# Kernel tuning notes

Measured on AMD Instinct MI355X. Metric: run time of the kernel, lower is better.

The kernel has to match this reference:

```python
import jax, jax.numpy as jnp
import numpy as np

SR = 11025.0
NYQ = SR / 2.0
N_OSC = 128
UP_LEN = 24576          # smooth_upsample2 target
TOTAL_SAMPLES = 16384   # noise-bank samples
WINDOW = 32             # (17 - 1) * 2
HOP = 16
FRAMES = 1024
CROP = 4096

# buffers derived from zounds.GeometricScale(20, nyquist-20, 0.05, 128)
CENTERS = jnp.asarray(np.geomspace(20.0, NYQ - 20.0, N_OSC), dtype=jnp.float32)
ERBS = CENTERS * 0.108 + 24.7


def conv1d(x, w, pad):
    # x: [B, Cin, T], w: [Cout, Cin, K]
    return jax.lax.conv_general_dilated(
        x, w, window_strides=(1,), padding=[(pad, pad)],
        dimension_numbers=('NCH', 'OIH', 'NCH'))


def lrelu(x):
    return jax.nn.leaky_relu(x, 0.2)


def setup_inputs() -> dict:
    key = jax.random.key(0)
    ks = jax.random.split(key, 16)
    d = {}
    d['x'] = jax.random.normal(ks[0], (16, 256, 64), jnp.float32)
    # xavier-ish scales: std ~ sqrt(2/(fan_in+fan_out))
    d['w_main0'] = jax.random.normal(ks[1], (512, 256, 1), jnp.float32) * 0.06
    d['w_main1'] = jax.random.normal(ks[2], (512, 512, 3), jnp.float32) * 0.03
    d['w_main2'] = jax.random.normal(ks[3], (512, 512, 3), jnp.float32) * 0.03
    d['w_main3'] = jax.random.normal(ks[4], (512, 512, 3), jnp.float32) * 0.03
    d['w_freq'] = jax.random.normal(ks[5], (256, 512, 1), jnp.float32) * 0.06
    for i in range(4):
        d[f'w_nl{i}'] = jax.random.normal(ks[6 + i], (512, 512, 7), jnp.float32) * 0.02
        d[f'b_nl{i}'] = jnp.zeros((512,), jnp.float32)
    d['w_noise_loud'] = jax.random.normal(ks[10], (17, 512, 1), jnp.float32) * 0.06
    d['noise'] = jax.random.uniform(ks[11], (16, FRAMES, WINDOW), jnp.float32)  # mapped to (-1,1) inside
    return d


def reference(x, w_main0, w_main1, w_main2, w_main3, w_freq,
              w_nl0, b_nl0, w_nl1, b_nl1, w_nl2, b_nl2, w_nl3, b_nl3,
              w_noise_loud, noise):
    B = x.shape[0]
    # ---- main conv stack (all bias-free, leaky_relu 0.2) ----
    h = lrelu(conv1d(x, w_main0, 0))
    h = lrelu(conv1d(h, w_main1, 1))
    h = lrelu(conv1d(h, w_main2, 1))
    h = lrelu(conv1d(h, w_main3, 1))          # [B, 512, 64]

    # ---- per-oscillator loudness & frequency ----
    osc = conv1d(h, w_freq, 0)                # [B, 256, 64]
    l = osc[:, :N_OSC, :] ** 2
    f = jnp.tanh(osc[:, N_OSC:, :]) * 0.5
    f = CENTERS[None, :, None] + f * ERBS[None, :, None]

    y = h
    for w, b in ((w_nl0, b_nl0), (w_nl1, b_nl1), (w_nl2, b_nl2), (w_nl3, b_nl3)):
        y = jnp.repeat(y, 2, axis=-1)
        y = lrelu(conv1d(y, w, 3) + b[None, :, None])
    n_l = conv1d(y, w_noise_loud, 0) ** 2     # [B, 17, 1024]

    # ---- smooth (linear) upsample of loudness/frequency envelopes ----
    l_up = jax.image.resize(l, (B, N_OSC, UP_LEN), 'linear')
    f_up = jax.image.resize(f, (B, N_OSC, UP_LEN), 'linear')

    # ---- oscillator bank: clamp, phase cumsum, sin, amp-weighted reduce ----
    f_up = jnp.clip(f_up, 20.0, NYQ)
    phases = jnp.cumsum(f_up * (2.0 * jnp.pi / SR), axis=-1)   # [B,128,24576]
    harmonic = jnp.sum(jnp.sin(phases) * l_up, axis=1, keepdims=True)  # [B,1,24576]

    # ---- noise bank: FFT-filter per-frame white noise, overlap-add ----
    nz = noise * 2.0 - 1.0                    # uniform(-1,1), [B, 1024, 32]
    coeffs = jnp.fft.rfft(nz, norm='ortho') * n_l.transpose(0, 2, 1)  # [B,1024,17]
    frames_sig = jnp.fft.irfft(coeffs, n=WINDOW, norm='ortho')        # [B,1024,32]
    pos = HOP * jnp.arange(FRAMES)[:, None] + jnp.arange(WINDOW)[None, :]
    buf = jnp.zeros((B, HOP * (FRAMES - 1) + WINDOW), jnp.float32)
    buf = buf.at[:, pos].add(frames_sig)
    noise_sig = buf[:, :TOTAL_SAMPLES][:, None, :]            # [B,1,16384]
    noise_full = jnp.pad(noise_sig, ((0, 0), (0, 0), (CROP, CROP)))

    sig = harmonic + noise_full
    sig = sig / (jnp.max(jnp.abs(sig), axis=(1, 2), keepdims=True) + 1e-8)
    return sig[:, :, CROP:-CROP]              # [B, 1, 16384]
```

## Files before the change

kernel.cpp:

```cpp
#include <hip/hip_runtime.h>
#include <cstdio>
#include <math.h>

#define NB 16
#define NC 512
#define T0 64
#define NOSC 128
#define UPLEN 24576
#define NTOT 16384
#define NWIN 32
#define NFRAMES 1024
#define NCROP 4096
#define NCHUNK 96
#define CHT 256

#define TWO_PI_D 6.283185307179586
#define INV_2PI_D 0.15915494309189535
#define K_PHASE (6.283185307179586/11025.0)

typedef unsigned short u16;
typedef short bf16x8 __attribute__((ext_vector_type(8)));
typedef short short8 __attribute__((ext_vector_type(8)));
typedef float f32x4 __attribute__((ext_vector_type(4)));

static __device__ __forceinline__ float lrelu_f(float x){ return x > 0.f ? x : 0.2f*x; }

static __device__ __forceinline__ u16 bf16_rne(float x){
  unsigned u = __float_as_uint(x);
  unsigned r = (u + 0x7FFFu + ((u >> 16) & 1u)) >> 16;
  return (u16)r;
}
static __device__ __forceinline__ void bf16_split(float x, u16& h, u16& l){
  h = bf16_rne(x);
  float hf = __uint_as_float(((unsigned)h) << 16);
  l = bf16_rne(x - hf);
}

__global__ void k_tables(float* __restrict__ centers, float* __restrict__ erbs){
  int o = threadIdx.x;
  if (o < NOSC){
    double lg0 = log10(20.0);
    double lg1 = log10(5492.5);
    double e = (o == NOSC-1) ? lg1 : (o*(lg1-lg0))/(double)(NOSC-1) + lg0;
    float c = (float)pow(10.0, e);
    centers[o] = c;
    erbs[o] = c*0.108f + 24.7f;
  }
}

__global__ __launch_bounds__(256) void k_conv1(const float* __restrict__ in, const float* __restrict__ w,
                                               float* __restrict__ out, int Cin, int Cout){
  int b = blockIdx.x;
  int lane = threadIdx.x & 63;
  int wv = __builtin_amdgcn_readfirstlane(threadIdx.x >> 6);
  int co0 = blockIdx.y*16 + wv*4;
  const float* inb = in + (size_t)b*Cin*T0 + lane;
  float a[2][4] = {{0,0,0,0},{0,0,0,0}};
  for (int ci = 0; ci < Cin; ci += 8){
    float v[8];
    #pragma unroll
    for (int u = 0; u < 8; ++u) v[u] = inb[(size_t)(ci+u)*T0];
    #pragma unroll
    for (int u = 0; u < 8; ++u)
      #pragma unroll
      for (int j = 0; j < 4; ++j)
        a[u&1][j] += v[u] * w[(size_t)(co0+j)*Cin + ci+u];
  }
  #pragma unroll
  for (int j = 0; j < 4; ++j)
    out[((size_t)b*Cout + co0 + j)*T0 + lane] = lrelu_f(a[0][j] + a[1][j]);
}

__global__ __launch_bounds__(256) void k_conv3(const float* __restrict__ in, const float* __restrict__ w,
                                               float* __restrict__ out){
  int b = blockIdx.x;
  int lane = threadIdx.x & 63;
  int wv = __builtin_amdgcn_readfirstlane(threadIdx.x >> 6);
  int co0 = blockIdx.y*16 + wv*4;
  const float* inb = in + (size_t)b*NC*T0 + lane;
  float a[2][4] = {{0,0,0,0},{0,0,0,0}};
  for (int ci = 0; ci < NC; ci += 8){
    float v[8];
    #pragma unroll
    for (int u = 0; u < 8; ++u) v[u] = inb[(size_t)(ci+u)*T0];
    #pragma unroll
    for (int u = 0; u < 8; ++u){
      float vm = __shfl_up(v[u], 1);
      float vp = __shfl_down(v[u], 1);
      if (lane == 0) vm = 0.f;
      if (lane == 63) vp = 0.f;
      #pragma unroll
      for (int j = 0; j < 4; ++j){
        const float* wp = w + ((size_t)(co0+j)*NC + ci+u)*3;
        a[u&1][j] += wp[0]*vm + wp[1]*v[u] + wp[2]*vp;
      }
    }
  }
  #pragma unroll
  for (int j = 0; j < 4; ++j)
    out[((size_t)b*NC + co0 + j)*T0 + lane] = lrelu_f(a[0][j] + a[1][j]);
}

__global__ __launch_bounds__(256) void k_freq(const float* __restrict__ h, const float* __restrict__ w,
                                              const float* __restrict__ centers, const float* __restrict__ erbs,
                                              float* __restrict__ l_buf, float* __restrict__ f_buf){
  int b = blockIdx.x;
  int lane = threadIdx.x & 63;
  int wv = __builtin_amdgcn_readfirstlane(threadIdx.x >> 6);
  int o0 = blockIdx.y*16 + wv*4;
  const float* hb = h + (size_t)b*NC*T0 + lane;
  double a[2][4] = {{0,0,0,0},{0,0,0,0}};
  for (int ci = 0; ci < NC; ci += 8){
    float v[8];
    #pragma unroll
    for (int u = 0; u < 8; ++u) v[u] = hb[(size_t)(ci+u)*T0];
    #pragma unroll
    for (int u = 0; u < 8; ++u)
      #pragma unroll
      for (int j = 0; j < 4; ++j)
        a[u&1][j] += (double)v[u] * (double)w[(size_t)(o0+j)*NC + ci+u];
  }
  #pragma unroll
  for (int j = 0; j < 4; ++j){
    double av = a[0][j] + a[1][j];
    int o = o0 + j;
    if (o < NOSC){
      l_buf[((size_t)b*NOSC + o)*T0 + lane] = (float)(av*av);
    } else {
      int oo = o - NOSC;
      double fv = (double)centers[oo] + tanh(av)*0.5*(double)erbs[oo];
      f_buf[((size_t)b*NOSC + oo)*T0 + lane] = (float)fv;
    }
  }
}

__global__ __launch_bounds__(256) void k_prepw3(const float* __restrict__ w, u16* __restrict__ Wh, u16* __restrict__ Wl){
  int gid = blockIdx.x*256 + threadIdx.x;
  int co = gid >> 6;
  int ci0 = (gid & 63)*8;
  float tv[8][8];
  #pragma unroll
  for (int j = 0; j < 8; ++j){
    const float* wp = w + ((size_t)co*NC + ci0 + j)*7;
    float w0=wp[0],w1=wp[1],w2=wp[2],w3=wp[3],w4=wp[4],w5=wp[5],w6=wp[6];
    tv[0][j]=w0;    tv[1][j]=w1+w2; tv[2][j]=w3+w4; tv[3][j]=w5+w6;
    tv[4][j]=w0+w1; tv[5][j]=w2+w3; tv[6][j]=w4+w5; tv[7][j]=w6;
  }
  int cot = co >> 4, r16 = co & 15, cik = ci0 >> 5, kg = (ci0 >> 3) & 3;
  #pragma unroll
  for (int tap = 0; tap < 8; ++tap){
    short8 h8, l8;
    #pragma unroll
    for (int j = 0; j < 8; ++j){ u16 h,l; bf16_split(tv[tap][j],h,l); h8[j]=(short)h; l8[j]=(short)l; }
    size_t o = (((size_t)tap*32 + cot)*16 + cik)*512 + r16*32 + kg*8;
    *(short8*)(Wh+o) = h8;
    *(short8*)(Wl+o) = l8;
  }
}

__global__ __launch_bounds__(256) void k_prepb3(const float* __restrict__ in, u16* __restrict__ Bh,
                                                u16* __restrict__ Bl, int Tin){
  __shared__ float lds[32][65];
  int t0 = blockIdx.x*64, cik = blockIdx.y, b = blockIdx.z;
  int ci0 = cik*32;
  int tid = threadIdx.x;
  if (blockIdx.x == 0 && tid < 128){
    int rr = tid >> 5, ci = tid & 31;
    int row = (rr < 2) ? rr : Tin + rr;
    size_t o = (((size_t)b*16 + cik)*(Tin+4) + row)*32 + ci;
    Bh[o] = 0;
    if (Bl) Bl[o] = 0;
  }
  #pragma unroll
  for (int u = 0; u < 2; ++u){
    int v = tid + u*256;
    int ci = v >> 4, tc = (v & 15)*4;
    float4 x = *(const float4*)(in + ((size_t)b*NC + ci0 + ci)*Tin + t0 + tc);
    lds[ci][tc]=x.x; lds[ci][tc+1]=x.y; lds[ci][tc+2]=x.z; lds[ci][tc+3]=x.w;
  }
  __syncthreads();
  int r = tid >> 2, g = tid & 3;
  short8 h8, l8;
  #pragma unroll
  for (int j = 0; j < 8; ++j){
    u16 h,l; bf16_split(lds[g*8+j][r], h, l);
    h8[j]=(short)h; l8[j]=(short)l;
  }
  size_t o = (((size_t)b*16 + cik)*(Tin+4) + 2 + t0 + r)*32 + g*8;
  *(short8*)(Bh+o) = h8;
  if (Bl) *(short8*)(Bl+o) = l8;
}

__global__ __launch_bounds__(256) void k_combprep(const float* __restrict__ pbuf, const float* __restrict__ bias,
                                                  u16* __restrict__ Bh, u16* __restrict__ Bl, int Tout, int KS){
  __shared__ float lds[32][65];
  int t0 = blockIdx.x*64, cik = blockIdx.y, b = blockIdx.z;
  int ci0 = cik*32;
  int tid = threadIdx.x;
  const size_t slab = (size_t)NB*NC*Tout;
  if (blockIdx.x == 0 && tid < 128){
    int rr = tid >> 5, ci = tid & 31;
    int row = (rr < 2) ? rr : Tout + rr;
    size_t o = (((size_t)b*16 + cik)*(Tout+4) + row)*32 + ci;
    Bh[o] = 0;
    if (Bl) Bl[o] = 0;
  }
  #pragma unroll
  for (int u = 0; u < 2; ++u){
    int v = tid + u*256;
    int ci = v >> 4, tc = (v & 15)*4;
    size_t base = ((size_t)b*NC + ci0 + ci)*Tout + t0 + tc;
    float4 s = make_float4(0.f, 0.f, 0.f, 0.f);
    for (int ks = 0; ks < KS; ++ks){
      float4 x = *(const float4*)(pbuf + (size_t)ks*slab + base);
      s.x += x.x; s.y += x.y; s.z += x.z; s.w += x.w;
    }
    float bv = bias[ci0 + ci];
    lds[ci][tc]   = lrelu_f(s.x + bv);
    lds[ci][tc+1] = lrelu_f(s.y + bv);
    lds[ci][tc+2] = lrelu_f(s.z + bv);
    lds[ci][tc+3] = lrelu_f(s.w + bv);
  }
  __syncthreads();
  int r = tid >> 2, g = tid & 3;
  short8 h8, l8;
  #pragma unroll
  for (int j = 0; j < 8; ++j){
    u16 h,l; bf16_split(lds[g*8+j][r], h, l);
    h8[j]=(short)h; l8[j]=(short)l;
  }
  size_t o = (((size_t)b*16 + cik)*(Tout+4) + 2 + t0 + r)*32 + g*8;
  *(short8*)(Bh+o) = h8;
  if (Bl) *(short8*)(Bl+o) = l8;
}

template<bool FINAL, bool USEBL>
__global__ __launch_bounds__(128, 2) void k_nlmfma7(const u16* __restrict__ Wh, const u16* __restrict__ Wl,
                                                    const u16* __restrict__ Bh, const u16* __restrict__ Bl,
                                                    const float* __restrict__ bias, float* __restrict__ outp,
                                                    int Tin, int KS, int tsh, int nper){
  const int lane = threadIdx.x & 63;
  const int wv = __builtin_amdgcn_readfirstlane(threadIdx.x >> 6);
  const int r16 = lane & 15, kg = lane >> 4;
  const int bid = blockIdx.x;
  const int co_t = (bid & 7) >> 1;
  const int idx = (bid & 1)*nper + (bid >> 3);
  const int Tt = 1 << tsh;
  const int t_t = idx & (Tt - 1);
  const int zb = idx >> tsh;
  const int b  = zb & (NB-1);
  const int ks = zb >> 4;
  const int coT0 = co_t*8 + wv*4;
  const int t_w  = t_t*64;
  const int cikBeg = (ks * (NC / KS)) >> 5;
  const int cikEnd = cikBeg + ((NC / KS) >> 5);

  f32x4 acc[2][4][4];
  f32x4 zz = {0.f, 0.f, 0.f, 0.f};
  #pragma unroll
  for (int p = 0; p < 2; ++p)
    #pragma unroll
    for (int c = 0; c < 4; ++c)
      #pragma unroll
      for (int f = 0; f < 4; ++f) acc[p][c][f] = zz;

  const int laneOff = r16*32 + kg*8;

  for (int cik = cikBeg; cik < cikEnd; ++cik){
    const size_t bBase = (((size_t)b*16 + cik)*(Tin+4) + t_w + r16)*32 + kg*8;
    #pragma unroll
    for (int s = 0; s < 5; ++s){
      bf16x8 bh[4], bl[4];
      #pragma unroll
      for (int f = 0; f < 4; ++f){
        bh[f] = *(const bf16x8*)(Bh + bBase + (size_t)(s + f*16)*32);
        if (USEBL) bl[f] = *(const bf16x8*)(Bl + bBase + (size_t)(s + f*16)*32);
      }
      #pragma unroll
      for (int e = 0; e < 2; ++e){
        if ((e == 0 && s < 4) || (e == 1 && s >= 1)){
          const int tap = (e == 0) ? s : (3 + s);
          bf16x8 ah[4], al[4];
          #pragma unroll
          for (int c = 0; c < 4; ++c){
            size_t ao = (((size_t)tap*32 + coT0 + c)*16 + cik)*512 + laneOff;
            ah[c] = *(const bf16x8*)(Wh + ao);
            al[c] = *(const bf16x8*)(Wl + ao);
          }
          #pragma unroll
          for (int c = 0; c < 4; ++c){
            #pragma unroll
            for (int f = 0; f < 4; ++f){
              f32x4 a = acc[e][c][f];
              a = __builtin_amdgcn_mfma_f32_16x16x32_bf16(ah[c], bh[f], a, 0, 0, 0);
              if (USEBL)
                a = __builtin_amdgcn_mfma_f32_16x16x32_bf16(ah[c], bl[f], a, 0, 0, 0);
              a = __builtin_amdgcn_mfma_f32_16x16x32_bf16(al[c], bh[f], a, 0, 0, 0);
              acc[e][c][f] = a;
            }
          }
        }
      }
    }
  }

  const int Tout = 2*Tin;
  const size_t slab = (size_t)NB*NC*Tout;
  const int co_w = co_t*128 + wv*64;
  #pragma unroll
  for (int c = 0; c < 4; ++c){
    #pragma unroll
    for (int r = 0; r < 4; ++r){
      int co = co_w + c*16 + kg*4 + r;
      #pragma unroll
      for (int f = 0; f < 4; ++f){
        int t = t_w + f*16 + r16;
        if (FINAL){
          float bv = bias[co];
          float2 v;
          v.x = lrelu_f(acc[0][c][f][r] + bv);
          v.y = lrelu_f(acc[1][c][f][r] + bv);
          *(float2*)(outp + ((size_t)b*NC + co)*Tout + 2*t) = v;
        } else {
          float2 v;
          v.x = acc[0][c][f][r];
          v.y = acc[1][c][f][r];
          *(float2*)(outp + (size_t)ks*slab + ((size_t)b*NC + co)*Tout + 2*t) = v;
        }
      }
    }
  }
}

__global__ __launch_bounds__(256) void k_nlout(const float* __restrict__ y3, const float* __restrict__ w,
                                               float* __restrict__ n_l){
  int b = blockIdx.y;
  int j = blockIdx.x*256 + threadIdx.x;
  float acc[17];
  #pragma unroll
  for (int k = 0; k < 17; ++k) acc[k] = 0.f;
  const float* yb = y3 + (size_t)b*NC*NFRAMES + j;
  for (int ci = 0; ci < NC; ++ci){
    float v = yb[(size_t)ci*NFRAMES];
    #pragma unroll
    for (int k = 0; k < 17; ++k) acc[k] += v * w[k*NC + ci];
  }
  #pragma unroll
  for (int k = 0; k < 17; ++k)
    n_l[((size_t)b*17 + k)*NFRAMES + j] = acc[k]*acc[k];
}

__global__ __launch_bounds__(256) void k_nlout3(const float* __restrict__ pbuf, const float* __restrict__ w,
                                                const float* __restrict__ bias, float* __restrict__ qbuf, int KS){
  int b = blockIdx.y;
  int cs = blockIdx.z;
  int j = blockIdx.x*256 + threadIdx.x;
  const size_t slab = (size_t)NB*NC*NFRAMES;
  const size_t slabQ = (size_t)NB*17*NFRAMES;
  float acc[17];
  #pragma unroll
  for (int k = 0; k < 17; ++k) acc[k] = 0.f;
  const float* pb = pbuf + (size_t)b*NC*NFRAMES + j;
  int ci0 = cs*64;
  for (int ci = ci0; ci < ci0 + 64; ++ci){
    float s = pb[(size_t)ci*NFRAMES];
    for (int ks = 1; ks < KS; ++ks) s += pb[(size_t)ks*slab + (size_t)ci*NFRAMES];
    float v = lrelu_f(s + bias[ci]);
    #pragma unroll
    for (int k = 0; k < 17; ++k) acc[k] += v * w[k*NC + ci];
  }
  #pragma unroll
  for (int k = 0; k < 17; ++k)
    qbuf[(size_t)cs*slabQ + ((size_t)b*17 + k)*NFRAMES + j] = acc[k];
}

__global__ __launch_bounds__(256) void k_nlsq(const float* __restrict__ qbuf, float* __restrict__ n_l){
  size_t e = (size_t)blockIdx.x*256 + threadIdx.x;
  const size_t slabQ = (size_t)NB*17*NFRAMES;
  float s = 0.f;
  #pragma unroll
  for (int cs = 0; cs < 8; ++cs) s += qbuf[(size_t)cs*slabQ + e];
  n_l[e] = s*s;
}

__global__ __launch_bounds__(256) void k_noise(const float* __restrict__ noise, const float* __restrict__ n_l,
                                               float* __restrict__ frames){
  __shared__ float ctab[NWIN], stab[NWIN];
  int tid = threadIdx.x;
  if (tid < NWIN){
    double ang = (TWO_PI_D/NWIN)*tid;
    ctab[tid] = (float)cos(ang);
    stab[tid] = (float)sin(ang);
  }
  __syncthreads();
  int j = blockIdx.x*256 + tid;
  int b = blockIdx.y;
  const float* src = noise + ((size_t)b*NFRAMES + j)*NWIN;
  float nz[NWIN];
  #pragma unroll
  for (int n = 0; n < NWIN; ++n) nz[n] = src[n]*2.f - 1.f;
  float y[NWIN];
  #pragma unroll
  for (int n = 0; n < NWIN; ++n) y[n] = 0.f;
  const float* g = n_l + (size_t)b*17*NFRAMES + j;
  for (int k = 0; k < 17; ++k){
    float A = 0.f, Bv = 0.f;
    int m = 0;
    #pragma unroll
    for (int n = 0; n < NWIN; ++n){
      A  += nz[n]*ctab[m];
      Bv += nz[n]*stab[m];
      m = (m + k) & (NWIN-1);
    }
    float gk = g[(size_t)k*NFRAMES];
    float sc = (k == 0 || k == 16) ? 1.f : 2.f;
    float ga = sc*gk*A, gb = sc*gk*Bv;
    m = 0;
    #pragma unroll
    for (int n = 0; n < NWIN; ++n){
      y[n] += ga*ctab[m] + gb*stab[m];
      m = (m + k) & (NWIN-1);
    }
  }
  float* dst = frames + ((size_t)b*NFRAMES + j)*NWIN;
  #pragma unroll
  for (int n = 0; n < NWIN; ++n) dst[n] = y[n] * (1.f/NWIN);
}

__global__ __launch_bounds__(256) void k_chunksum(const float* __restrict__ f_buf, double* __restrict__ cb){
  int idx = blockIdx.x*256 + threadIdx.x;
  int bo = idx & (NB*NOSC - 1);
  int c  = idx >> 11;
  const float* f = f_buf + (size_t)bo*T0;
  double s = 0.0;
  int t0 = c*CHT;
  int cached = -1000; float f0 = 0.f, f1 = 0.f;
  for (int i = 0; i < CHT; ++i){
    int t = t0 + i;
    double coord = (t + 0.5)*(1.0/384.0) - 0.5;
    double fl = floor(coord);
    int lo = (int)fl;
    float wfr = (float)(coord - fl);
    if (lo != cached){
      cached = lo;
      int i0 = lo < 0 ? 0 : (lo > 63 ? 63 : lo);
      int i1 = lo+1 < 0 ? 0 : (lo+1 > 63 ? 63 : lo+1);
      f0 = f[i0]; f1 = f[i1];
    }
    float v = f0*(1.f - wfr) + f1*wfr;
    v = fminf(fmaxf(v, 20.f), 5512.5f);
    s += (double)v;
  }
  cb[(size_t)bo*NCHUNK + c] = s;
}

__global__ void k_scan(double* __restrict__ cb){
  int bo = blockIdx.x*64 + threadIdx.x;
  if (bo < NB*NOSC){
    double* p = cb + (size_t)bo*NCHUNK;
    double run = 0.0;
    for (int c = 0; c < NCHUNK; ++c){ double v = p[c]; p[c] = run; run += v; }
  }
}

__global__ __launch_bounds__(128) void k_osc(const float* __restrict__ f_buf, const float* __restrict__ l_buf,
                                             const double* __restrict__ cb, const float* __restrict__ frames,
                                             float* __restrict__ sig){
  int c = blockIdx.x;
  int b = blockIdx.y;
  int o = threadIdx.x;
  __shared__ float tile[64*129];
  __shared__ float harm[256];
  __shared__ float red[128];
  const float* f = f_buf + ((size_t)b*NOSC + o)*T0;
  const float* l = l_buf + ((size_t)b*NOSC + o)*T0;
  double sum = cb[((size_t)b*NOSC + o)*NCHUNK + c];
  int tstart = c*CHT;
  int cached = -1000; float f0 = 0.f, f1 = 0.f, l0 = 0.f, l1 = 0.f;
  for (int sub = 0; sub < 4; ++sub){
    for (int i = 0; i < 64; ++i){
      int t = tstart + sub*64 + i;
      double coord = (t + 0.5)*(1.0/384.0) - 0.5;
      double fl = floor(coord);
      int lo = (int)fl;
      float wfr = (float)(coord - fl);
      if (lo != cached){
        cached = lo;
        int i0 = lo < 0 ? 0 : (lo > 63 ? 63 : lo);
        int i1 = lo+1 < 0 ? 0 : (lo+1 > 63 ? 63 : lo+1);
        f0 = f[i0]; f1 = f[i1]; l0 = l[i0]; l1 = l[i1];
      }
      float fv = f0*(1.f - wfr) + f1*wfr;
      fv = fminf(fmaxf(fv, 20.f), 5512.5f);
      float lv = l0*(1.f - wfr) + l1*wfr;
      sum += (double)fv;
      double ph = sum * K_PHASE;
      double q = floor(ph * INV_2PI_D);
      float phw = (float)(ph - q*TWO_PI_D);
      tile[i*129 + o] = sinf(phw) * lv;
    }
    __syncthreads();
    {
      int row = o & 63, half = o >> 6;
      float s = 0.f;
      const float* tp = tile + row*129 + half*64;
      for (int j = 0; j < 64; ++j) s += tp[j];
      red[row*2 + half] = s;
    }
    __syncthreads();
    if (o < 64) harm[sub*64 + o] = red[o*2] + red[o*2 + 1];
    __syncthreads();
  }
  for (int i = o; i < CHT; i += 128){
    int t = tstart + i;
    float v = harm[i];
    int tn = t - NCROP;
    if (tn >= 0 && tn < NTOT){
      int j1 = tn >> 4, n1 = tn & 15;
      float nv = frames[((size_t)b*NFRAMES + j1)*NWIN + n1];
      if (j1 > 0) nv += frames[((size_t)b*NFRAMES + j1 - 1)*NWIN + n1 + 16];
      v += nv;
    }
    sig[(size_t)b*UPLEN + t] = v;
  }
}

__global__ __launch_bounds__(256) void k_max(const float* __restrict__ sig, float* __restrict__ maxa){
  int b = blockIdx.x;
  float m = 0.f;
  for (int i = threadIdx.x; i < UPLEN; i += 256)
    m = fmaxf(m, fabsf(sig[(size_t)b*UPLEN + i]));
  #pragma unroll
  for (int off = 32; off > 0; off >>= 1)
    m = fmaxf(m, __shfl_xor(m, off, 64));
  __shared__ float sm[4];
  if ((threadIdx.x & 63) == 0) sm[threadIdx.x >> 6] = m;
  __syncthreads();
  if (threadIdx.x == 0)
    maxa[b] = fmaxf(fmaxf(sm[0], sm[1]), fmaxf(sm[2], sm[3]));
}

__global__ __launch_bounds__(256) void k_final(const float* __restrict__ sig, const float* __restrict__ maxa,
                                               float* __restrict__ out){
  int b = blockIdx.y;
  int i = blockIdx.x*256 + threadIdx.x;
  out[(size_t)b*NTOT + i] = sig[(size_t)b*UPLEN + NCROP + i] / (maxa[b] + 1e-8f);
}

extern "C" void kernel_launch(void* const* d_in, const int* in_sizes, int n_in,
                              void* d_out, int out_size, void* d_ws, size_t ws_size,
                              hipStream_t stream)
{
  (void)in_sizes; (void)n_in;
  const float* x     = (const float*)d_in[0];
  const float* w0    = (const float*)d_in[1];
  const float* w1    = (const float*)d_in[2];
  const float* w2    = (const float*)d_in[3];
  const float* w3    = (const float*)d_in[4];
  const float* wf    = (const float*)d_in[5];
  const float* wnl[4] = {(const float*)d_in[6], (const float*)d_in[8], (const float*)d_in[10], (const float*)d_in[12]};
  const float* bnl[4] = {(const float*)d_in[7], (const float*)d_in[9], (const float*)d_in[11], (const float*)d_in[13]};
  const float* wno   = (const float*)d_in[14];
  const float* noise = (const float*)d_in[15];
  float* out = (float*)d_out;

  char* base = (char*)d_ws;
  size_t off = 0;
  auto carve = [&](size_t bytes) -> void* {
    void* r = base + off;
    off += (bytes + 255) & ~(size_t)255;
    return r;
  };
  double* cbase  = (double*)carve(sizeof(double)*(size_t)NB*NOSC*NCHUNK);
  float* h_a     = (float*)carve(4ull*NB*NC*T0);
  float* h_b     = (float*)carve(4ull*NB*NC*T0);
  float* l_buf   = (float*)carve(4ull*NB*NOSC*T0);
  float* f_buf   = (float*)carve(4ull*NB*NOSC*T0);
  float* Vbuf    = (float*)carve(4ull*NB*NC*512);
  float* Ubuf    = (float*)carve(4ull*NB*NC*1024);
  float* n_l     = (float*)carve(4ull*NB*17*NFRAMES);
  float* frames  = (float*)carve(4ull*NB*NFRAMES*NWIN);
  float* sig     = (float*)carve(4ull*NB*UPLEN);
  float* maxa    = (float*)carve(4ull*NB);
  float* centers = (float*)carve(4ull*NOSC);
  float* erbs    = (float*)carve(4ull*NOSC);
  float* Qbuf    = (float*)carve(4ull*8*NB*17*NFRAMES);
  u16* Wh        = (u16*)carve(2ull*8*NC*NC);
  u16* Wl        = (u16*)carve(2ull*8*NC*NC);
  u16* Bh        = (u16*)carve(2ull*NB*(512+4)*NC);
  if (off > ws_size){
    fprintf(stderr, "kernel_launch: workspace too small: need %zu bytes, have %zu\n", off, ws_size);
    return;
  }
  u16* Bl = nullptr;
  size_t blBytes = ((2ull*NB*(512+4)*NC) + 255) & ~(size_t)255;
  if (off + blBytes <= ws_size){
    Bl = (u16*)carve(2ull*NB*(512+4)*NC);
  } else {
    fprintf(stderr, "kernel_launch: B-lo buffer dropped (ws %zu), using single-bf16 activations\n", ws_size);
  }
  float* Pbuf = nullptr;
  int ksL[4] = {1, 1, 1, 1};
  bool l4Fused = false;
  {
    size_t t1 = ((4ull*NB*NC*2048) + 255) & ~(size_t)255;
    size_t t2 = ((4ull*NB*NC*1024) + 255) & ~(size_t)255;
    if (off + t1 <= ws_size){
      Pbuf = (float*)carve(4ull*NB*NC*2048);
      ksL[0] = 16; ksL[1] = 8; ksL[2] = 4; ksL[3] = 2;
      l4Fused = true;
    } else if (off + t2 <= ws_size){
      Pbuf = (float*)carve(4ull*NB*NC*1024);
      ksL[0] = 8; ksL[1] = 4; ksL[2] = 2; ksL[3] = 1;
      fprintf(stderr, "kernel_launch: Pbuf tier2 (ws %zu)\n", ws_size);
    } else {
      fprintf(stderr, "kernel_launch: Pbuf dropped (ws %zu), K-split disabled\n", ws_size);
    }
  }
  if (out_size != NB*NTOT){
    fprintf(stderr, "kernel_launch: unexpected out_size %d (want %d)\n", out_size, NB*NTOT);
  }

  k_tables<<<1, 128, 0, stream>>>(centers, erbs);

  k_conv1<<<dim3(NB, 32), 256, 0, stream>>>(x, w0, h_a, 256, 512);
  k_conv3<<<dim3(NB, 32), 256, 0, stream>>>(h_a, w1, h_b);
  k_conv3<<<dim3(NB, 32), 256, 0, stream>>>(h_b, w2, h_a);
  k_conv3<<<dim3(NB, 32), 256, 0, stream>>>(h_a, w3, h_b);

  k_freq<<<dim3(NB, 16), 256, 0, stream>>>(h_b, wf, centers, erbs, l_buf, f_buf);

  auto launch_mfma = [&](int Tin, int KS, float* dst, const float* bias, bool final_){
    int Tt = Tin/64; if (Tt < 1) Tt = 1;
    int tsh = __builtin_ctz(Tt);
    int nblk = 4 * Tt * NB * KS;
    int nper = (Tt * NB * KS) / 2;
    if (final_){
      if (Bl) k_nlmfma7<true, true ><<<dim3(nblk), 128, 0, stream>>>(Wh, Wl, Bh, Bl, bias, dst, Tin, KS, tsh, nper);
      else    k_nlmfma7<true, false><<<dim3(nblk), 128, 0, stream>>>(Wh, Wl, Bh, nullptr, bias, dst, Tin, KS, tsh, nper);
    } else {
      if (Bl) k_nlmfma7<false, true ><<<dim3(nblk), 128, 0, stream>>>(Wh, Wl, Bh, Bl, bias, dst, Tin, KS, tsh, nper);
      else    k_nlmfma7<false, false><<<dim3(nblk), 128, 0, stream>>>(Wh, Wl, Bh, nullptr, bias, dst, Tin, KS, tsh, nper);
    }
  };

  const int TinL[4] = {64, 128, 256, 512};
  if (Pbuf){
    k_prepw3<<<dim3(128), 256, 0, stream>>>(wnl[0], Wh, Wl);
    k_prepb3<<<dim3(1, 16, NB), 256, 0, stream>>>(h_b, Bh, Bl, 64);
    for (int L = 0; L < 3; ++L){
      int Tin = TinL[L], Tout = 2*Tin;
      launch_mfma(Tin, ksL[L], Pbuf, nullptr, false);
      k_prepw3<<<dim3(128), 256, 0, stream>>>(wnl[L+1], Wh, Wl);
      k_combprep<<<dim3(Tout/64, 16, NB), 256, 0, stream>>>(Pbuf, bnl[L], Bh, Bl, Tout, ksL[L]);
    }
    if (l4Fused){
      launch_mfma(512, ksL[3], Pbuf, nullptr, false);
      k_nlout3<<<dim3(4, NB, 8), 256, 0, stream>>>(Pbuf, wno, bnl[3], Qbuf, ksL[3]);
      k_nlsq<<<dim3((NB*17*NFRAMES)/256), 256, 0, stream>>>(Qbuf, n_l);
    } else {
      launch_mfma(512, 1, Ubuf, bnl[3], true);
      k_nlout<<<dim3(4, NB), 256, 0, stream>>>(Ubuf, wno, n_l);
    }
  } else {
    const float* srcs[4] = {h_b, Vbuf, Ubuf, Vbuf};
    float* dsts[4] = {Vbuf, Ubuf, Vbuf, Ubuf};
    for (int L = 0; L < 4; ++L){
      int Tin = TinL[L];
      k_prepw3<<<dim3(128), 256, 0, stream>>>(wnl[L], Wh, Wl);
      k_prepb3<<<dim3(Tin/64, 16, NB), 256, 0, stream>>>(srcs[L], Bh, Bl, Tin);
      launch_mfma(Tin, 1, dsts[L], bnl[L], true);
    }
    k_nlout<<<dim3(4, NB), 256, 0, stream>>>(Ubuf, wno, n_l);
  }

  k_noise<<<dim3(4, NB), 256, 0, stream>>>(noise, n_l, frames);

  k_chunksum<<<dim3((NB*NOSC*NCHUNK)/256), 256, 0, stream>>>(f_buf, cbase);
  k_scan<<<dim3(32), 64, 0, stream>>>(cbase);
  k_osc<<<dim3(NCHUNK, NB), 128, 0, stream>>>(f_buf, l_buf, cbase, frames, sig);

  k_max<<<dim3(NB), 256, 0, stream>>>(sig, maxa);
  k_final<<<dim3(NTOT/256, NB), 256, 0, stream>>>(sig, maxa, out);
}
```

Before: 943.3 us.

## Halve oscillator chunk size, table-drive interpolation indices, use fast sine

Halves the oscillator chunk length and doubles the chunk count, so the phase-accumulation kernels launch twice as many blocks. The per-sample double-precision floor and coordinate math is replaced by a precomputed table of packed interpolation indices and weights. The block-local reduction becomes a 4-way split over 32-row tiles. The accurate sinf becomes __sinf, which cuts transcendental cost but may lose accuracy on the range-reduced phase.

```diff
diff --git a/kernel.cpp b/kernel.cpp
--- a/kernel.cpp
+++ b/kernel.cpp
@@ -11,8 +11,8 @@
 #define NWIN 32
 #define NFRAMES 1024
 #define NCROP 4096
-#define NCHUNK 96
-#define CHT 256
+#define NCHUNK 192
+#define CHT 128
 
 #define TWO_PI_D 6.283185307179586
 #define INV_2PI_D 0.15915494309189535
@@ -45,6 +45,20 @@
     float c = (float)pow(10.0, e);
     centers[o] = c;
     erbs[o] = c*0.108f + 24.7f;
+  }
+}
+
+__global__ __launch_bounds__(256) void k_ttab(int* __restrict__ tti, float* __restrict__ ttw){
+  int t = blockIdx.x*256 + threadIdx.x;
+  if (t < UPLEN){
+    double coord = (t + 0.5)*(1.0/384.0) - 0.5;
+    double fl = floor(coord);
+    int lo = (int)fl;
+    float w = (float)(coord - fl);
+    int i0 = lo < 0 ? 0 : (lo > 63 ? 63 : lo);
+    int i1 = lo+1 < 0 ? 0 : (lo+1 > 63 ? 63 : lo+1);
+    tti[t] = i0 | (i1 << 16);
+    ttw[t] = w;
   }
 }
 
@@ -427,27 +441,20 @@
   for (int n = 0; n < NWIN; ++n) dst[n] = y[n] * (1.f/NWIN);
 }
 
-__global__ __launch_bounds__(256) void k_chunksum(const float* __restrict__ f_buf, double* __restrict__ cb){
+__global__ __launch_bounds__(256) void k_chunksum(const float* __restrict__ f_buf, const int* __restrict__ tti,
+                                                  const float* __restrict__ ttw, double* __restrict__ cb){
   int idx = blockIdx.x*256 + threadIdx.x;
   int bo = idx & (NB*NOSC - 1);
   int c  = idx >> 11;
   const float* f = f_buf + (size_t)bo*T0;
   double s = 0.0;
   int t0 = c*CHT;
-  int cached = -1000; float f0 = 0.f, f1 = 0.f;
   for (int i = 0; i < CHT; ++i){
     int t = t0 + i;
-    double coord = (t + 0.5)*(1.0/384.0) - 0.5;
-    double fl = floor(coord);
-    int lo = (int)fl;
-    float wfr = (float)(coord - fl);
-    if (lo != cached){
-      cached = lo;
-      int i0 = lo < 0 ? 0 : (lo > 63 ? 63 : lo);
-      int i1 = lo+1 < 0 ? 0 : (lo+1 > 63 ? 63 : lo+1);
-      f0 = f[i0]; f1 = f[i1];
-    }
-    float v = f0*(1.f - wfr) + f1*wfr;
+    int ii = tti[t];
+    float w = ttw[t];
+    float f0 = f[ii & 0xFFFF], f1 = f[ii >> 16];
+    float v = f0*(1.f - w) + f1*w;
     v = fminf(fmaxf(v, 20.f), 5512.5f);
     s += (double)v;
   }
@@ -464,56 +471,50 @@
 }
 
 __global__ __launch_bounds__(128) void k_osc(const float* __restrict__ f_buf, const float* __restrict__ l_buf,
-                                             const double* __restrict__ cb, const float* __restrict__ frames,
+                                             const double* __restrict__ cb, const int* __restrict__ tti,
+                                             const float* __restrict__ ttw, const float* __restrict__ frames,
                                              float* __restrict__ sig){
   int c = blockIdx.x;
   int b = blockIdx.y;
   int o = threadIdx.x;
-  __shared__ float tile[64*129];
-  __shared__ float harm[256];
-  __shared__ float red[128];
+  __shared__ float tile[32*129];
+  __shared__ float harm[CHT];
+  __shared__ float red[32][4];
   const float* f = f_buf + ((size_t)b*NOSC + o)*T0;
   const float* l = l_buf + ((size_t)b*NOSC + o)*T0;
   double sum = cb[((size_t)b*NOSC + o)*NCHUNK + c];
   int tstart = c*CHT;
-  int cached = -1000; float f0 = 0.f, f1 = 0.f, l0 = 0.f, l1 = 0.f;
   for (int sub = 0; sub < 4; ++sub){
-    for (int i = 0; i < 64; ++i){
-      int t = tstart + sub*64 + i;
-      double coord = (t + 0.5)*(1.0/384.0) - 0.5;
-      double fl = floor(coord);
-      int lo = (int)fl;
-      float wfr = (float)(coord - fl);
-      if (lo != cached){
-        cached = lo;
-        int i0 = lo < 0 ? 0 : (lo > 63 ? 63 : lo);
-        int i1 = lo+1 < 0 ? 0 : (lo+1 > 63 ? 63 : lo+1);
-        f0 = f[i0]; f1 = f[i1]; l0 = l[i0]; l1 = l[i1];
-      }
-      float fv = f0*(1.f - wfr) + f1*wfr;
+    for (int i = 0; i < 32; ++i){
+      int t = tstart + sub*32 + i;
+      int ii = tti[t];
+      float w = ttw[t];
+      int i0 = ii & 0xFFFF, i1 = ii >> 16;
+      float fv = f[i0]*(1.f - w) + f[i1]*w;
       fv = fminf(fmaxf(fv, 20.f), 5512.5f);
-      float lv = l0*(1.f - wfr) + l1*wfr;
+      float lv = l[i0]*(1.f - w) + l[i1]*w;
       sum += (double)fv;
       double ph = sum * K_PHASE;
       double q = floor(ph * INV_2PI_D);
       float phw = (float)(ph - q*TWO_PI_D);
-      tile[i*129 + o] = sinf(phw) * lv;
+      tile[i*129 + o] = __sinf(phw) * lv;
     }
     __syncthreads();
     {
-      int row = o & 63, half = o >> 6;
+      int r = o & 31, qd = o >> 5;
       float s = 0.f;
-      const float* tp = tile + row*129 + half*64;
-      for (int j = 0; j < 64; ++j) s += tp[j];
-      red[row*2 + half] = s;
+      const float* tp = tile + r*129 + qd*32;
+      #pragma unroll
+      for (int j = 0; j < 32; ++j) s += tp[j];
+      red[r][qd] = s;
     }
     __syncthreads();
-    if (o < 64) harm[sub*64 + o] = red[o*2] + red[o*2 + 1];
+    if (o < 32) harm[sub*32 + o] = (red[o][0] + red[o][1]) + (red[o][2] + red[o][3]);
     __syncthreads();
   }
-  for (int i = o; i < CHT; i += 128){
-    int t = tstart + i;
-    float v = harm[i];
+  {
+    int t = tstart + o;
+    float v = harm[o];
     int tn = t - NCROP;
     if (tn >= 0 && tn < NTOT){
       int j1 = tn >> 4, n1 = tn & 15;
@@ -584,6 +585,8 @@
   float* maxa    = (float*)carve(4ull*NB);
   float* centers = (float*)carve(4ull*NOSC);
   float* erbs    = (float*)carve(4ull*NOSC);
+  int*   tti     = (int*)carve(4ull*UPLEN);
+  float* ttw     = (float*)carve(4ull*UPLEN);
   float* Qbuf    = (float*)carve(4ull*8*NB*17*NFRAMES);
   u16* Wh        = (u16*)carve(2ull*8*NC*NC);
   u16* Wl        = (u16*)carve(2ull*8*NC*NC);
@@ -622,6 +625,7 @@
   }
 
   k_tables<<<1, 128, 0, stream>>>(centers, erbs);
+  k_ttab<<<dim3(UPLEN/256), 256, 0, stream>>>(tti, ttw);
 
   k_conv1<<<dim3(NB, 32), 256, 0, stream>>>(x, w0, h_a, 256, 512);
   k_conv3<<<dim3(NB, 32), 256, 0, stream>>>(h_a, w1, h_b);
@@ -676,9 +680,9 @@
 
   k_noise<<<dim3(4, NB), 256, 0, stream>>>(noise, n_l, frames);
 
-  k_chunksum<<<dim3((NB*NOSC*NCHUNK)/256), 256, 0, stream>>>(f_buf, cbase);
+  k_chunksum<<<dim3((NB*NOSC*NCHUNK)/256), 256, 0, stream>>>(f_buf, tti, ttw, cbase);
   k_scan<<<dim3(32), 64, 0, stream>>>(cbase);
-  k_osc<<<dim3(NCHUNK, NB), 128, 0, stream>>>(f_buf, l_buf, cbase, frames, sig);
+  k_osc<<<dim3(NCHUNK, NB), 128, 0, stream>>>(f_buf, l_buf, cbase, tti, ttw, frames, sig);
 
   k_max<<<dim3(NB), 256, 0, stream>>>(sig, maxa);
   k_final<<<dim3(NTOT/256, NB), 256, 0, stream>>>(sig, maxa, out);
```

After: 1.349 ms. 1.43x slower.
